# Optimization experiments

Measured on AMD Instinct MI355X. Metric: run time of the kernel, lower is better.

The kernel has to match this reference:

```python
import jax, jax.numpy as jnp
import numpy as np

B, C, H, W = 4, 512, 64, 64
CK = C // 8  # key/query channels


def setup_inputs() -> dict:
    key = jax.random.key(0)
    ks = jax.random.split(key, 4)
    x = jax.random.normal(ks[0], (B, C, H, W), dtype=jnp.float32)
    # 1x1 conv weights -> plain [out, in] matrices; fan-in scaled like torch default-ish
    Wf = jax.random.normal(ks[1], (CK, C), dtype=jnp.float32) * (1.0 / np.sqrt(C))
    Wg = jax.random.normal(ks[2], (CK, C), dtype=jnp.float32) * (1.0 / np.sqrt(C))
    Wh = jax.random.normal(ks[3], (C, C), dtype=jnp.float32) * (1.0 / np.sqrt(C))
    bf = jnp.zeros((CK,), dtype=jnp.float32)
    bg = jnp.zeros((CK,), dtype=jnp.float32)
    bh = jnp.zeros((C,), dtype=jnp.float32)
    gamma = jnp.zeros((1,), dtype=jnp.float32)
    return {"x": x, "Wf": Wf, "bf": bf, "Wg": Wg, "bg": bg, "Wh": Wh, "bh": bh, "gamma": gamma}


def reference(x, Wf, bf, Wg, bg, Wh, bh, gamma):
    b, c, h, w = x.shape
    n = h * w
    xf = x.reshape(b, c, n)  # [B, C, N]
    # 1x1 convs == per-pixel linear maps
    f = jnp.einsum('kc,bcn->bkn', Wf, xf) + bf[None, :, None]  # [B, CK, N]
    g = jnp.einsum('kc,bcn->bkn', Wg, xf) + bg[None, :, None]  # [B, CK, N]
    hx = jnp.einsum('oc,bcn->bon', Wh, xf) + bh[None, :, None]  # [B, C, N]
    # energy[b,i,j] = sum_k f[b,k,i] * g[b,k,j]  (f_x.permute(0,2,1) @ g_x)
    energy = jnp.einsum('bki,bkj->bij', f, g)  # [B, N, N]
    attention = jax.nn.softmax(energy, axis=-1)
    # out[b,c,i] = sum_j hx[b,c,j] * attention[b,i,j]  (h_x @ attention^T)
    out = jnp.einsum('bcj,bij->bci', hx, attention)  # [B, C, N]
    out = out.reshape(b, c, h, w)
    return gamma[0] * out + x
```

## Files before the change

### kernel.cpp

```cpp
#include <hip/hip_runtime.h>
#include <hip/hip_bf16.h>

#define NB 4
#define CC 512
#define NN 4096
#define CKK 64
#define NT 32

typedef _Float16 f16x4 __attribute__((ext_vector_type(4)));
typedef _Float16 f16x8 __attribute__((ext_vector_type(8)));
typedef float    f32x4 __attribute__((ext_vector_type(4)));

#define BAR()       asm volatile("s_barrier" ::: "memory")
#define BAR_LGKM()  asm volatile("s_waitcnt lgkmcnt(0)\n\ts_barrier" ::: "memory")
#define BAR_VM(n)   asm volatile("s_waitcnt vmcnt(" #n ")\n\ts_barrier" ::: "memory")

__device__ __forceinline__ void g2l16(const _Float16* g, _Float16* l) {
    __builtin_amdgcn_global_load_lds(
        (const __attribute__((address_space(1))) void*)g,
        (__attribute__((address_space(3))) void*)l, 16, 0, 0);
}

__device__ __forceinline__ void stage_tile(const _Float16* __restrict__ g, int ldg,
                                           _Float16* lds, int lane, int wave) {
    #pragma unroll
    for (int r = 0; r < 2; r++) {
        int q = r * 4 + wave;
        int row = q * 16 + (lane >> 2);
        int col = (lane & 3) * 8;
        g2l16(g + (size_t)row * ldg + col, lds + q * 512 + lane * 8);
    }
}

__device__ __forceinline__ void stage_swz(const _Float16* __restrict__ g, int ldg,
                                          _Float16* lds, int tid) {
    int row = tid >> 2;
    int scq = (tid & 3) ^ ((row >> 1) & 3);
    g2l16(g + (size_t)row * ldg + scq * 8, lds + tid * 8);
}

__device__ __forceinline__ f16x8 rd_swz(const _Float16* lds, int row, int quad) {
    int q = quad ^ ((row >> 1) & 3);
    return *(const f16x8*)(lds + row * 32 + q * 8);
}

__launch_bounds__(256)
__global__ void prep(const float* __restrict__ x, _Float16* __restrict__ xT,
                     const float* __restrict__ Wf, const float* __restrict__ bf_,
                     const float* __restrict__ Wg, const float* __restrict__ bg_,
                     const float* __restrict__ Wh, const float* __restrict__ bh_,
                     _Float16* __restrict__ Wall, float* __restrict__ Ball) {
    const int N = NN, C = CC;
    int bid = blockIdx.x;
    int t = threadIdx.x;
    if (bid < 2048) {
        int n0 = (bid & 63) << 6;
        int c0 = ((bid >> 6) & 7) << 6;
        int b  = bid >> 9;
        __shared__ float T[64][65];
        const float* xb = x + (size_t)b * C * N;
        #pragma unroll
        for (int r = 0; r < 4; r++) {
            int c = (t >> 4) + 16 * r;
            int n4 = (t & 15) * 4;
            float4 v = *(const float4*)(xb + (size_t)(c0 + c) * N + n0 + n4);
            T[n4 + 0][c] = v.x; T[n4 + 1][c] = v.y; T[n4 + 2][c] = v.z; T[n4 + 3][c] = v.w;
        }
        __syncthreads();
        int n = t >> 2, cb = (t & 3) * 16;
        f16x8 h0, h1;
        #pragma unroll
        for (int i = 0; i < 8; i++) { h0[i] = (_Float16)T[n][cb + i]; h1[i] = (_Float16)T[n][cb + 8 + i]; }
        _Float16* dst = xT + (size_t)b * N * C + (size_t)(n0 + n) * C + c0 + cb;
        *(f16x8*)dst = h0;
        *(f16x8*)(dst + 8) = h1;
    } else {
        int o = bid - 2048;
        const float* src;
        if (o < 64)       src = Wf + (size_t)o * C;
        else if (o < 128) src = Wg + (size_t)(o - 64) * C;
        else              src = Wh + (size_t)(o - 128) * C;
        Wall[(size_t)o * C + t]       = (_Float16)src[t];
        Wall[(size_t)o * C + 256 + t] = (_Float16)src[256 + t];
        if (t == 0)
            Ball[o] = (o < 64) ? bf_[o] : (o < 128 ? bg_[o - 64] : bh_[o - 128]);
    }
}

__launch_bounds__(256)
__global__ void proj_mfma(const _Float16* __restrict__ xT, const _Float16* __restrict__ Wall,
                          const float* __restrict__ Ball,
                          _Float16* __restrict__ Ft, _Float16* __restrict__ Gt,
                          _Float16* __restrict__ Hx) {
    const int N = NN, C = CC;
    int n0 = blockIdx.x * 128;
    int o0 = blockIdx.y * 128;
    int b  = blockIdx.z;
    const _Float16* Arow = Wall + (size_t)o0 * C;
    const _Float16* Brow = xT + (size_t)b * N * C + (size_t)n0 * C;
    __shared__ _Float16 As[128 * 32];
    __shared__ _Float16 Bs[128 * 32];
    int tid = threadIdx.x, lane = tid & 63, wave = tid >> 6;
    int wm = wave & 1, wn = wave >> 1, lrow = lane & 15, quad = lane >> 4;
    f32x4 acc[4][4] = {};
    for (int kc = 0; kc < C; kc += 32) {
        __syncthreads();
        stage_tile(Arow + kc, C, As, lane, wave);
        stage_tile(Brow + kc, C, Bs, lane, wave);
        __syncthreads();
        f16x8 af[4], bf[4];
        #pragma unroll
        for (int mi = 0; mi < 4; mi++)
            af[mi] = *(const f16x8*)(As + (wm * 64 + mi * 16 + lrow) * 32 + quad * 8);
        #pragma unroll
        for (int ni = 0; ni < 4; ni++)
            bf[ni] = *(const f16x8*)(Bs + (wn * 64 + ni * 16 + lrow) * 32 + quad * 8);
        #pragma unroll
        for (int mi = 0; mi < 4; mi++)
            #pragma unroll
            for (int ni = 0; ni < 4; ni++)
                acc[mi][ni] = __builtin_amdgcn_mfma_f32_16x16x32_f16(af[mi], bf[ni], acc[mi][ni], 0, 0, 0);
    }
    float bias_r[4][4];
    #pragma unroll
    for (int mi = 0; mi < 4; mi++)
        #pragma unroll
        for (int r = 0; r < 4; r++)
            bias_r[mi][r] = Ball[o0 + wm * 64 + mi * 16 + quad * 4 + r];
    _Float16* Ftb = Ft + (size_t)b * NN * CKK;
    _Float16* Gtb = Gt + (size_t)b * NN * CKK;
    _Float16* Hxb = Hx + (size_t)b * CC * N;
    #pragma unroll
    for (int mi = 0; mi < 4; mi++)
        #pragma unroll
        for (int ni = 0; ni < 4; ni++) {
            int o = o0 + wm * 64 + mi * 16 + quad * 4;
            int n = n0 + wn * 64 + ni * 16 + lrow;
            f16x4 v;
            #pragma unroll
            for (int r = 0; r < 4; r++) v[r] = (_Float16)(acc[mi][ni][r] + bias_r[mi][r]);
            if (o < 64)       *(f16x4*)(Ftb + (size_t)n * CKK + o) = v;
            else if (o < 128) *(f16x4*)(Gtb + (size_t)n * CKK + (o - 64)) = v;
            else {
                #pragma unroll
                for (int r = 0; r < 4; r++)
                    Hxb[(size_t)(o - 128 + r) * N + n] = v[r];
            }
        }
}

#define PST_LD  136
#define MRL     9
#define SM_FT    0
#define SM_BSG   16384
#define SM_PST   49152
#define SM_AH    83968
#define SM_MRED  149504
#define SM_MRUN  154112
#define SM_LRUN  154624
#define SM_OSC   155136
#define SM_FLAG  155648
#define SM_TOTAL 155776

__launch_bounds__(512, 2)
__global__ void attn_fused(const _Float16* __restrict__ Ft, const _Float16* __restrict__ Gt,
                           const _Float16* __restrict__ Hx, const float* __restrict__ x,
                           const float* __restrict__ gamma, float* __restrict__ out) {
    const int N = NN;
    extern __shared__ char smem[];
    _Float16* FtL  = (_Float16*)(smem + SM_FT);
    _Float16* BsGp = (_Float16*)(smem + SM_BSG);
    _Float16* Pst  = (_Float16*)(smem + SM_PST);
    _Float16* AhL  = (_Float16*)(smem + SM_AH);
    float* Mred = (float*)(smem + SM_MRED);
    float* Mrun = (float*)(smem + SM_MRUN);
    float* Lrun = (float*)(smem + SM_LRUN);
    float* Osc  = (float*)(smem + SM_OSC);
    int*   Fl   = (int*)(smem + SM_FLAG);

    const int b  = blockIdx.z;
    const int i0 = blockIdx.x * 128;
    const int c0 = blockIdx.y * 256;
    const int tid = threadIdx.x;
    const int lane = tid & 63, w = tid >> 6;
    const int lrow = lane & 15, quad = lane >> 4;
    const int wi = w & 3, wj = w >> 2;
    const int wc = w >> 1, wi2 = w & 1;

    const _Float16* Ftb = Ft + (size_t)b * N * CKK + (size_t)i0 * CKK;
    const _Float16* Gtb = Gt + (size_t)b * N * CKK;
    const _Float16* Hxb = Hx + (size_t)b * CC * N + (size_t)c0 * N;

    stage_swz(Ftb,      CKK, FtL,        tid);
    stage_swz(Ftb + 32, CKK, FtL + 4096, tid);
    stage_swz(Gtb,      CKK, BsGp,        tid);
    stage_swz(Gtb + 32, CKK, BsGp + 4096, tid);
    if (tid < 128) { Mrun[tid] = -1e30f; Lrun[tid] = 0.0f; }
    if (tid == 0) Fl[0] = 0;
    __syncthreads();

    f16x8 afs[2][2];
    #pragma unroll
    for (int mi = 0; mi < 2; mi++)
        #pragma unroll
        for (int ks = 0; ks < 2; ks++)
            afs[mi][ks] = rd_swz(FtL + ks * 4096, wi * 32 + mi * 16 + lrow, quad);

    f32x4 acc[4][4] = {};

    #pragma unroll 1
    for (int jt = 0; jt < NT; jt++) {
        const int cur = jt & 1;
        const _Float16* Hxr = Hxb + (size_t)jt * 128;
        stage_swz(Hxr,                        N, AhL,         tid);
        stage_swz(Hxr + (size_t)128 * N,      N, AhL + 4096,  tid);
        stage_swz(Hxr + 32,                   N, AhL + 8192,  tid);
        stage_swz(Hxr + 32 + (size_t)128 * N, N, AhL + 12288, tid);
        stage_swz(Hxr + 64,                   N, AhL + 16384, tid);
        stage_swz(Hxr + 64 + (size_t)128 * N, N, AhL + 20480, tid);
        stage_swz(Hxr + 96,                   N, AhL + 24576, tid);
        stage_swz(Hxr + 96 + (size_t)128 * N, N, AhL + 28672, tid);
        const _Float16* Gn = Gtb + (size_t)((jt + 1) & (NT - 1)) * 128 * CKK;
        _Float16* Gdst = BsGp + (cur ^ 1) * 8192;
        stage_swz(Gn,      CKK, Gdst,        tid);
        stage_swz(Gn + 32, CKK, Gdst + 4096, tid);
        BAR_VM(10);

        const _Float16* Bst = BsGp + cur * 8192;
        f32x4 sacc[2][4] = {};
        #pragma unroll
        for (int ks = 0; ks < 2; ks++)
            #pragma unroll
            for (int ni = 0; ni < 4; ni++) {
                f16x8 bfs = rd_swz(Bst + ks * 4096, wj * 64 + ni * 16 + lrow, quad);
                #pragma unroll
                for (int mi = 0; mi < 2; mi++)
                    sacc[mi][ni] = __builtin_amdgcn_mfma_f32_16x16x32_f16(afs[mi][ks], bfs, sacc[mi][ni], 0, 0, 0);
            }
        float red[8];
        #pragma unroll
        for (int mi = 0; mi < 2; mi++)
            #pragma unroll
            for (int r = 0; r < 4; r++)
                red[mi * 4 + r] = fmaxf(fmaxf(sacc[mi][0][r], sacc[mi][1][r]),
                                        fmaxf(sacc[mi][2][r], sacc[mi][3][r]));
        #pragma unroll
        for (int off = 1; off < 8; off <<= 1)
            #pragma unroll
            for (int s = 0; s < 8; s++)
                red[s] = fmaxf(red[s], __shfl_xor(red[s], off));
        if ((lrow & 7) == 0) {
            #pragma unroll
            for (int mi = 0; mi < 2; mi++)
                #pragma unroll
                for (int r = 0; r < 4; r++)
                    Mred[(wi * 32 + mi * 16 + quad * 4 + r) * MRL + wj * 2 + (lrow >> 3)] = red[mi * 4 + r];
        }
        BAR_LGKM();

        if (tid < 128) {
            const float* mr = Mred + tid * MRL;
            float mt = mr[0];
            #pragma unroll
            for (int k = 1; k < 8; k++) mt = fmaxf(mt, mr[k]);
            float mo = Mrun[tid];
            if (mt > mo) {
                Fl[0] = 1;
                Mrun[tid] = mt;
                float sc = __expf(mo - mt);
                Osc[tid] = sc;
                Lrun[tid] *= sc;
            } else {
                Osc[tid] = 1.0f;
            }
        }
        BAR_LGKM();

        #pragma unroll
        for (int mi = 0; mi < 2; mi++)
            #pragma unroll
            for (int r = 0; r < 4; r++) {
                int row = wi * 32 + mi * 16 + quad * 4 + r;
                float m = Mrun[row];
                float ls = 0.f;
                #pragma unroll
                for (int ni = 0; ni < 4; ni++) {
                    _Float16 p16 = (_Float16)__expf(sacc[mi][ni][r] - m);
                    Pst[row * PST_LD + wj * 64 + ni * 16 + lrow] = p16;
                    ls += (float)p16;
                }
                red[mi * 4 + r] = ls;
            }
        #pragma unroll
        for (int off = 1; off < 8; off <<= 1)
            #pragma unroll
            for (int s = 0; s < 8; s++)
                red[s] += __shfl_xor(red[s], off);
        if ((lrow & 7) == 0) {
            #pragma unroll
            for (int mi = 0; mi < 2; mi++)
                #pragma unroll
                for (int r = 0; r < 4; r++)
                    Mred[(wi * 32 + mi * 16 + quad * 4 + r) * MRL + wj * 2 + (lrow >> 3)] = red[mi * 4 + r];
        }
        if (Fl[0]) {
            float scv[4];
            #pragma unroll
            for (int ni = 0; ni < 4; ni++) scv[ni] = Osc[wi2 * 64 + ni * 16 + lrow];
            #pragma unroll
            for (int mi = 0; mi < 4; mi++)
                #pragma unroll
                for (int ni = 0; ni < 4; ni++)
                    #pragma unroll
                    for (int r = 0; r < 4; r++)
                        acc[mi][ni][r] *= scv[ni];
        }
        BAR_LGKM();

        if (tid < 128) {
            const float* mr = Mred + tid * MRL;
            float s = 0.f;
            #pragma unroll
            for (int k = 0; k < 8; k++) s += mr[k];
            Lrun[tid] += s;
        }
        if (tid == 0) Fl[0] = 0;

        auto pv_half = [&](const _Float16* Ab, int kb) {
            #pragma unroll
            for (int ks2 = 0; ks2 < 2; ks2++) {
                f16x8 bfv[4];
                #pragma unroll
                for (int ni = 0; ni < 4; ni++)
                    bfv[ni] = *(const f16x8*)(Pst + (wi2 * 64 + ni * 16 + lrow) * PST_LD + (kb + ks2) * 32 + quad * 8);
                #pragma unroll
                for (int mi = 0; mi < 4; mi++) {
                    f16x8 av = rd_swz(Ab + ks2 * 8192, wc * 64 + mi * 16 + lrow, quad);
                    #pragma unroll
                    for (int ni = 0; ni < 4; ni++)
                        acc[mi][ni] = __builtin_amdgcn_mfma_f32_16x16x32_f16(av, bfv[ni], acc[mi][ni], 0, 0, 0);
                }
            }
        };
        BAR_VM(6);
        pv_half(AhL, 0);
        BAR_VM(2);
        pv_half(AhL + 16384, 2);
        BAR();
    }

    __syncthreads();
    if (tid < 128) Osc[tid] = 1.0f / Lrun[tid];
    __syncthreads();

    float gv = gamma[0];
    const float* xb = x + (size_t)b * CC * N;
    float* ob = out + (size_t)b * CC * N;
    float li[4];
    #pragma unroll
    for (int ni = 0; ni < 4; ni++) li[ni] = Osc[wi2 * 64 + ni * 16 + lrow];
    #pragma unroll
    for (int mi = 0; mi < 4; mi++)
        #pragma unroll
        for (int ni = 0; ni < 4; ni++)
            #pragma unroll
            for (int r = 0; r < 4; r++) {
                int c = c0 + wc * 64 + mi * 16 + quad * 4 + r;
                int i = i0 + wi2 * 64 + ni * 16 + lrow;
                ob[(size_t)c * N + i] = gv * (acc[mi][ni][r] * li[ni]) + xb[(size_t)c * N + i];
            }
}

extern "C" void kernel_launch(void* const* d_in, const int* in_sizes, int n_in,
                              void* d_out, int out_size, void* d_ws, size_t ws_size,
                              hipStream_t stream) {
    const float* x     = (const float*)d_in[0];
    const float* Wf    = (const float*)d_in[1];
    const float* bf    = (const float*)d_in[2];
    const float* Wg    = (const float*)d_in[3];
    const float* bg    = (const float*)d_in[4];
    const float* Wh    = (const float*)d_in[5];
    const float* bh    = (const float*)d_in[6];
    const float* gamma = (const float*)d_in[7];
    float* out = (float*)d_out;

    char* wsb = (char*)d_ws;
    _Float16* Wall = (_Float16*)wsb;
    float*    Ball = (float*)(wsb + ((size_t)768 << 10));
    _Float16* Ft = (_Float16*)(wsb + ((size_t)1 << 20));
    _Float16* Gt = (_Float16*)(wsb + ((size_t)3 << 20));
    _Float16* Hx = (_Float16*)(wsb + ((size_t)5 << 20));
    _Float16* xT = (_Float16*)(wsb + ((size_t)21 << 20));

    static const bool attn_attr_once = [] {
        hipFuncSetAttribute((const void*)attn_fused,
                            hipFuncAttributeMaxDynamicSharedMemorySize, SM_TOTAL);
        return true;
    }();
    (void)attn_attr_once;

    prep<<<dim3(2048 + 640), dim3(256), 0, stream>>>(
        x, xT, Wf, bf, Wg, bg, Wh, bh, Wall, Ball);
    proj_mfma<<<dim3(NN / 128, 5, NB), dim3(256), 0, stream>>>(xT, Wall, Ball, Ft, Gt, Hx);
    attn_fused<<<dim3(NN / 128, CC / 256, NB), dim3(512), SM_TOTAL, stream>>>(
        Ft, Gt, Hx, x, gamma, out);
}
```

Baseline: 292.0 us.

## Halve query tile and shrink LDS footprint to fit four blocks per CU

```diff
diff --git a/kernel.cpp b/kernel.cpp
--- a/kernel.cpp
+++ b/kernel.cpp
@@ -10,10 +10,6 @@
 typedef _Float16 f16x4 __attribute__((ext_vector_type(4)));
 typedef _Float16 f16x8 __attribute__((ext_vector_type(8)));
 typedef float    f32x4 __attribute__((ext_vector_type(4)));
-
-#define BAR()       asm volatile("s_barrier" ::: "memory")
-#define BAR_LGKM()  asm volatile("s_waitcnt lgkmcnt(0)\n\ts_barrier" ::: "memory")
-#define BAR_VM(n)   asm volatile("s_waitcnt vmcnt(" #n ")\n\ts_barrier" ::: "memory")
 
 __device__ __forceinline__ void g2l16(const _Float16* g, _Float16* l) {
     __builtin_amdgcn_global_load_lds(
@@ -42,6 +38,18 @@
 __device__ __forceinline__ f16x8 rd_swz(const _Float16* lds, int row, int quad) {
     int q = quad ^ ((row >> 1) & 3);
     return *(const f16x8*)(lds + row * 32 + q * 8);
+}
+
+__device__ __forceinline__ void stage_ft(const _Float16* __restrict__ g, int ldg,
+                                         _Float16* lds, int tid) {
+    int row = tid >> 3;
+    int ch = (tid & 7) ^ (row & 7);
+    g2l16(g + (size_t)row * ldg + ch * 8, lds + tid * 8);
+}
+
+__device__ __forceinline__ f16x8 rd_ft(const _Float16* lds, int row, int qq) {
+    int ch = qq ^ (row & 7);
+    return *(const f16x8*)(lds + row * 64 + ch * 8);
 }
 
 __launch_bounds__(256)
@@ -150,53 +158,47 @@
 }
 
 #define PST_LD  136
-#define MRL     9
-#define SM_FT    0
-#define SM_BSG   16384
+#define MRL     21
+#define SM_AH    0
+#define SM_BSG   32768
 #define SM_PST   49152
-#define SM_AH    83968
-#define SM_MRED  149504
-#define SM_MRUN  154112
-#define SM_LRUN  154624
-#define SM_OSC   155136
-#define SM_FLAG  155648
-#define SM_TOTAL 155776
-
-__launch_bounds__(512, 2)
+#define SM_MRED  66560
+#define SM_MRUN  71936
+#define SM_LRUN  72192
+#define SM_OSC   72448
+#define SM_TOTAL 72704
+
+__launch_bounds__(512, 4)
 __global__ void attn_fused(const _Float16* __restrict__ Ft, const _Float16* __restrict__ Gt,
                            const _Float16* __restrict__ Hx, const float* __restrict__ x,
                            const float* __restrict__ gamma, float* __restrict__ out) {
     const int N = NN;
     extern __shared__ char smem[];
-    _Float16* FtL  = (_Float16*)(smem + SM_FT);
-    _Float16* BsGp = (_Float16*)(smem + SM_BSG);
-    _Float16* Pst  = (_Float16*)(smem + SM_PST);
-    _Float16* AhL  = (_Float16*)(smem + SM_AH);
+    _Float16* AhL = (_Float16*)(smem + SM_AH);
+    _Float16* BsG = (_Float16*)(smem + SM_BSG);
+    _Float16* Pst = (_Float16*)(smem + SM_PST);
     float* Mred = (float*)(smem + SM_MRED);
     float* Mrun = (float*)(smem + SM_MRUN);
     float* Lrun = (float*)(smem + SM_LRUN);
     float* Osc  = (float*)(smem + SM_OSC);
-    int*   Fl   = (int*)(smem + SM_FLAG);
 
     const int b  = blockIdx.z;
-    const int i0 = blockIdx.x * 128;
+    const int i0 = blockIdx.x * 64;
     const int c0 = blockIdx.y * 256;
     const int tid = threadIdx.x;
     const int lane = tid & 63, w = tid >> 6;
     const int lrow = lane & 15, quad = lane >> 4;
-    const int wi = w & 3, wj = w >> 2;
+    const int wi = w & 1, wj = w >> 1;
     const int wc = w >> 1, wi2 = w & 1;
 
     const _Float16* Ftb = Ft + (size_t)b * N * CKK + (size_t)i0 * CKK;
     const _Float16* Gtb = Gt + (size_t)b * N * CKK;
     const _Float16* Hxb = Hx + (size_t)b * CC * N + (size_t)c0 * N;
 
-    stage_swz(Ftb,      CKK, FtL,        tid);
-    stage_swz(Ftb + 32, CKK, FtL + 4096, tid);
-    stage_swz(Gtb,      CKK, BsGp,        tid);
-    stage_swz(Gtb + 32, CKK, BsGp + 4096, tid);
-    if (tid < 128) { Mrun[tid] = -1e30f; Lrun[tid] = 0.0f; }
-    if (tid == 0) Fl[0] = 0;
+    stage_ft(Ftb, CKK, AhL, tid);
+    stage_swz(Gtb,      CKK, BsG,        tid);
+    stage_swz(Gtb + 32, CKK, BsG + 4096, tid);
+    if (tid < 64) { Mrun[tid] = -1e30f; Lrun[tid] = 0.0f; }
     __syncthreads();
 
     f16x8 afs[2][2];
@@ -204,78 +206,66 @@
     for (int mi = 0; mi < 2; mi++)
         #pragma unroll
         for (int ks = 0; ks < 2; ks++)
-            afs[mi][ks] = rd_swz(FtL + ks * 4096, wi * 32 + mi * 16 + lrow, quad);
-
-    f32x4 acc[4][4] = {};
+            afs[mi][ks] = rd_ft(AhL, wi * 32 + mi * 16 + lrow, ks * 4 + quad);
+
+    f32x4 acc[4][2] = {};
 
     #pragma unroll 1
     for (int jt = 0; jt < NT; jt++) {
-        const int cur = jt & 1;
+        __syncthreads();
+        f32x4 sacc[2][2] = {};
+        #pragma unroll
+        for (int ks = 0; ks < 2; ks++) {
+            f16x8 bq[2];
+            #pragma unroll
+            for (int nj = 0; nj < 2; nj++)
+                bq[nj] = rd_swz(BsG + ks * 4096, wj * 32 + nj * 16 + lrow, quad);
+            #pragma unroll
+            for (int mi = 0; mi < 2; mi++)
+                #pragma unroll
+                for (int nj = 0; nj < 2; nj++)
+                    sacc[mi][nj] = __builtin_amdgcn_mfma_f32_16x16x32_f16(afs[mi][ks], bq[nj], sacc[mi][nj], 0, 0, 0);
+        }
         const _Float16* Hxr = Hxb + (size_t)jt * 128;
-        stage_swz(Hxr,                        N, AhL,         tid);
-        stage_swz(Hxr + (size_t)128 * N,      N, AhL + 4096,  tid);
-        stage_swz(Hxr + 32,                   N, AhL + 8192,  tid);
-        stage_swz(Hxr + 32 + (size_t)128 * N, N, AhL + 12288, tid);
-        stage_swz(Hxr + 64,                   N, AhL + 16384, tid);
-        stage_swz(Hxr + 64 + (size_t)128 * N, N, AhL + 20480, tid);
-        stage_swz(Hxr + 96,                   N, AhL + 24576, tid);
-        stage_swz(Hxr + 96 + (size_t)128 * N, N, AhL + 28672, tid);
-        const _Float16* Gn = Gtb + (size_t)((jt + 1) & (NT - 1)) * 128 * CKK;
-        _Float16* Gdst = BsGp + (cur ^ 1) * 8192;
-        stage_swz(Gn,      CKK, Gdst,        tid);
-        stage_swz(Gn + 32, CKK, Gdst + 4096, tid);
-        BAR_VM(10);
-
-        const _Float16* Bst = BsGp + cur * 8192;
-        f32x4 sacc[2][4] = {};
-        #pragma unroll
-        for (int ks = 0; ks < 2; ks++)
-            #pragma unroll
-            for (int ni = 0; ni < 4; ni++) {
-                f16x8 bfs = rd_swz(Bst + ks * 4096, wj * 64 + ni * 16 + lrow, quad);
-                #pragma unroll
-                for (int mi = 0; mi < 2; mi++)
-                    sacc[mi][ni] = __builtin_amdgcn_mfma_f32_16x16x32_f16(afs[mi][ks], bfs, sacc[mi][ni], 0, 0, 0);
-            }
+        stage_swz(Hxr,                   N, AhL,        tid);
+        stage_swz(Hxr + (size_t)128 * N, N, AhL + 4096, tid);
         float red[8];
         #pragma unroll
         for (int mi = 0; mi < 2; mi++)
             #pragma unroll
             for (int r = 0; r < 4; r++)
-                red[mi * 4 + r] = fmaxf(fmaxf(sacc[mi][0][r], sacc[mi][1][r]),
-                                        fmaxf(sacc[mi][2][r], sacc[mi][3][r]));
-        #pragma unroll
-        for (int off = 1; off < 8; off <<= 1)
+                red[mi * 4 + r] = fmaxf(sacc[mi][0][r], sacc[mi][1][r]);
+        #pragma unroll
+        for (int off = 1; off < 4; off <<= 1)
             #pragma unroll
             for (int s = 0; s < 8; s++)
                 red[s] = fmaxf(red[s], __shfl_xor(red[s], off));
-        if ((lrow & 7) == 0) {
+        if ((lrow & 3) == 0) {
             #pragma unroll
             for (int mi = 0; mi < 2; mi++)
                 #pragma unroll
                 for (int r = 0; r < 4; r++)
-                    Mred[(wi * 32 + mi * 16 + quad * 4 + r) * MRL + wj * 2 + (lrow >> 3)] = red[mi * 4 + r];
-        }
-        BAR_LGKM();
-
-        if (tid < 128) {
+                    Mred[(wi * 32 + mi * 16 + quad * 4 + r) * MRL + wj * 4 + (lrow >> 2)] = red[mi * 4 + r];
+        }
+        __syncthreads();
+        {
+            const _Float16* Gn = Gtb + (size_t)((jt + 1) & (NT - 1)) * 128 * CKK;
+            stage_swz(Gn,      CKK, BsG,        tid);
+            stage_swz(Gn + 32, CKK, BsG + 4096, tid);
+        }
+        if (tid < 64) {
             const float* mr = Mred + tid * MRL;
             float mt = mr[0];
             #pragma unroll
-            for (int k = 1; k < 8; k++) mt = fmaxf(mt, mr[k]);
+            for (int k = 1; k < 16; k++) mt = fmaxf(mt, mr[k]);
             float mo = Mrun[tid];
-            if (mt > mo) {
-                Fl[0] = 1;
-                Mrun[tid] = mt;
-                float sc = __expf(mo - mt);
-                Osc[tid] = sc;
-                Lrun[tid] *= sc;
-            } else {
-                Osc[tid] = 1.0f;
-            }
-        }
-        BAR_LGKM();
-
+            float mn = fmaxf(mo, mt);
+            float sc = __expf(mo - mn);
+            Mrun[tid] = mn;
+            Osc[tid] = sc;
+            Lrun[tid] *= sc;
+        }
+        __syncthreads();
         #pragma unroll
         for (int mi = 0; mi < 2; mi++)
             #pragma unroll
@@ -284,89 +274,87 @@
                 float m = Mrun[row];
                 float ls = 0.f;
                 #pragma unroll
-                for (int ni = 0; ni < 4; ni++) {
-                    _Float16 p16 = (_Float16)__expf(sacc[mi][ni][r] - m);
-                    Pst[row * PST_LD + wj * 64 + ni * 16 + lrow] = p16;
+                for (int nj = 0; nj < 2; nj++) {
+                    _Float16 p16 = (_Float16)__expf(sacc[mi][nj][r] - m);
+                    Pst[row * PST_LD + wj * 32 + nj * 16 + lrow] = p16;
                     ls += (float)p16;
                 }
                 red[mi * 4 + r] = ls;
             }
         #pragma unroll
-        for (int off = 1; off < 8; off <<= 1)
+        for (int off = 1; off < 4; off <<= 1)
             #pragma unroll
             for (int s = 0; s < 8; s++)
                 red[s] += __shfl_xor(red[s], off);
-        if ((lrow & 7) == 0) {
+        if ((lrow & 3) == 0) {
             #pragma unroll
             for (int mi = 0; mi < 2; mi++)
                 #pragma unroll
                 for (int r = 0; r < 4; r++)
-                    Mred[(wi * 32 + mi * 16 + quad * 4 + r) * MRL + wj * 2 + (lrow >> 3)] = red[mi * 4 + r];
-        }
-        if (Fl[0]) {
-            float scv[4];
-            #pragma unroll
-            for (int ni = 0; ni < 4; ni++) scv[ni] = Osc[wi2 * 64 + ni * 16 + lrow];
+                    Mred[(wi * 32 + mi * 16 + quad * 4 + r) * MRL + wj * 4 + (lrow >> 2)] = red[mi * 4 + r];
+        }
+        {
+            float scv[2];
+            #pragma unroll
+            for (int ni = 0; ni < 2; ni++) scv[ni] = Osc[wi2 * 32 + ni * 16 + lrow];
             #pragma unroll
             for (int mi = 0; mi < 4; mi++)
                 #pragma unroll
-                for (int ni = 0; ni < 4; ni++)
+                for (int ni = 0; ni < 2; ni++)
                     #pragma unroll
                     for (int r = 0; r < 4; r++)
                         acc[mi][ni][r] *= scv[ni];
         }
-        BAR_LGKM();
-
-        if (tid < 128) {
+        __syncthreads();
+        if (tid < 64) {
             const float* mr = Mred + tid * MRL;
             float s = 0.f;
             #pragma unroll
-            for (int k = 0; k < 8; k++) s += mr[k];
+            for (int k = 0; k < 16; k++) s += mr[k];
             Lrun[tid] += s;
         }
-        if (tid == 0) Fl[0] = 0;
-
-        auto pv_half = [&](const _Float16* Ab, int kb) {
-            #pragma unroll
-            for (int ks2 = 0; ks2 < 2; ks2++) {
-                f16x8 bfv[4];
-                #pragma unroll
-                for (int ni = 0; ni < 4; ni++)
-                    bfv[ni] = *(const f16x8*)(Pst + (wi2 * 64 + ni * 16 + lrow) * PST_LD + (kb + ks2) * 32 + quad * 8);
-                #pragma unroll
-                for (int mi = 0; mi < 4; mi++) {
-                    f16x8 av = rd_swz(Ab + ks2 * 8192, wc * 64 + mi * 16 + lrow, quad);
-                    #pragma unroll
-                    for (int ni = 0; ni < 4; ni++)
-                        acc[mi][ni] = __builtin_amdgcn_mfma_f32_16x16x32_f16(av, bfv[ni], acc[mi][ni], 0, 0, 0);
-                }
-            }
-        };
-        BAR_VM(6);
-        pv_half(AhL, 0);
-        BAR_VM(2);
-        pv_half(AhL + 16384, 2);
-        BAR();
+        #pragma unroll
+        for (int kk = 0; kk < 4; kk++) {
+            __syncthreads();
+            if (kk < 3) {
+                const _Float16* src = Hxr + (kk + 1) * 32;
+                _Float16* dst = AhL + ((kk + 1) & 1) * 8192;
+                stage_swz(src,                   N, dst,        tid);
+                stage_swz(src + (size_t)128 * N, N, dst + 4096, tid);
+            }
+            const _Float16* A = AhL + (kk & 1) * 8192;
+            f16x8 bfv[2];
+            #pragma unroll
+            for (int ni = 0; ni < 2; ni++)
+                bfv[ni] = *(const f16x8*)(Pst + (wi2 * 32 + ni * 16 + lrow) * PST_LD + kk * 32 + quad * 8);
+            #pragma unroll
+            for (int mi = 0; mi < 4; mi++) {
+                f16x8 av = rd_swz(A, wc * 64 + mi * 16 + lrow, quad);
+                #pragma unroll
+                for (int ni = 0; ni < 2; ni++)
+                    acc[mi][ni] = __builtin_amdgcn_mfma_f32_16x16x32_f16(av, bfv[ni], acc[mi][ni], 0, 0, 0);
+            }
+        }
     }
 
     __syncthreads();
-    if (tid < 128) Osc[tid] = 1.0f / Lrun[tid];
+    if (tid < 64) Osc[tid] = 1.0f / Lrun[tid];
     __syncthreads();
 
     float gv = gamma[0];
     const float* xb = x + (size_t)b * CC * N;
     float* ob = out + (size_t)b * CC * N;
-    float li[4];
-    #pragma unroll
-    for (int ni = 0; ni < 4; ni++) li[ni] = Osc[wi2 * 64 + ni * 16 + lrow];
+    float li[2];
+    #pragma unroll
+    for (int ni = 0; ni < 2; ni++) li[ni] = Osc[wi2 * 32 + ni * 16 + lrow];
     #pragma unroll
     for (int mi = 0; mi < 4; mi++)
         #pragma unroll
-        for (int ni = 0; ni < 4; ni++)
+        for (int ni = 0; ni < 2; ni++)
             #pragma unroll
             for (int r = 0; r < 4; r++) {
                 int c = c0 + wc * 64 + mi * 16 + quad * 4 + r;
-                int i = i0 + wi2 * 64 + ni * 16 + lrow;
+                int i = i0 + wi2 * 32 + ni * 16 + lrow;
                 ob[(size_t)c * N + i] = gv * (acc[mi][ni][r] * li[ni]) + xb[(size_t)c * N + i];
             }
 }
@@ -402,6 +390,6 @@
     prep<<<dim3(2048 + 640), dim3(256), 0, stream>>>(
         x, xT, Wf, bf, Wg, bg, Wh, bh, Wall, Ball);
     proj_mfma<<<dim3(NN / 128, 5, NB), dim3(256), 0, stream>>>(xT, Wall, Ball, Ft, Gt, Hx);
-    attn_fused<<<dim3(NN / 128, CC / 256, NB), dim3(512), SM_TOTAL, stream>>>(
+    attn_fused<<<dim3(NN / 64, CC / 256, NB), dim3(512), SM_TOTAL, stream>>>(
         Ft, Gt, Hx, x, gamma, out);
 }
```

Result: no change. 290.2 us (-0.6%).
